# Kernel optimization log

Measured on AMD Instinct MI355X. Metric: run time of the kernel, lower is better.

Reference implementation:

```python
import jax, jax.numpy as jnp
import numpy as np
import math

NAT = 192
RCUT = 6.0
RC_ANG = 4.0
RSN_RAD = 32
RSN_ANG = 8
THETAN = 8
WIDTH = 0.5
WIDTH_ANG = 0.5
ZETA = 8.0
R0 = 0.25
BOX = 12.0


def fcut(r, rc):
    # 0.5*(1+cos(pi*r/rc)) inside cutoff, 0 outside
    return jnp.where(r <= rc, 0.5 * (1.0 + jnp.cos(jnp.pi * r / rc)), 0.0)


def app_gaussian(x):
    # power-series approximation of exp(-x): (1/(1+x/64))^64
    a = 1.0 / (1.0 + x / 64.0 + 1e-8)
    a2 = a * a; a4 = a2 * a2; a8 = a4 * a4; a16 = a8 * a8; a32 = a16 * a16
    return a32 * a32


def setup_inputs() -> dict:
    key = jax.random.key(0)
    ks = jax.random.split(key, 8)
    positions = jax.random.uniform(ks[0], (NAT, 3), dtype=jnp.float32) * BOX
    species_enc = jax.random.uniform(ks[1], (NAT,), dtype=jnp.float32)
    feat = RSN_RAD + RSN_ANG * THETAN  # 96
    W1 = jax.random.normal(ks[2], (feat, 128), dtype=jnp.float32) * (1.0 / math.sqrt(feat))
    b1 = jnp.zeros((128,), jnp.float32)
    W2 = jax.random.normal(ks[3], (128, 128), dtype=jnp.float32) * (1.0 / math.sqrt(128))
    b2 = jnp.zeros((128,), jnp.float32)
    W3 = jax.random.normal(ks[4], (128, 1), dtype=jnp.float32) * (1.0 / math.sqrt(128))
    b3 = jnp.zeros((1,), jnp.float32)
    return {"positions": positions, "species_enc": species_enc,
            "W1": W1, "b1": b1, "W2": W2, "b2": b2, "W3": W3, "b3": b3}


def reference(positions, species_enc, W1, b1, W2, b2, W3, b3):
    nat = positions.shape[0]
    # pairwise displacements r_ij = pos_i - pos_j  (matches transposed tf code)
    rij = positions[:, None, :] - positions[None, :, :]            # [i,j,3]
    rnorm = jnp.sqrt(jnp.sum(rij * rij, axis=-1) + 1e-12)           # [i,j]

    # ---- radial descriptors ----
    Rs = R0 + jnp.arange(RSN_RAD, dtype=jnp.float32) * (RCUT - R0) / RSN_RAD
    gauss = app_gaussian(WIDTH * (rnorm[:, None, :] - Rs[None, :, None]) ** 2)  # [i,s,j]
    rad = jnp.sum(species_enc[None, None, :] * gauss * fcut(rnorm, RCUT)[:, None, :], axis=-1)  # [nat, RsN_rad]

    # ---- angular (triplet) descriptors ----
    inv = 1.0 / (rnorm + 1e-20)
    u = rij * inv[:, :, None]                                       # unit vectors [i,j,3]
    cosT = jnp.einsum('ijd,ikd->ijk', u, u)                         # [i,j,k]
    sinT = jnp.sqrt(jnp.clip(1.0 - cosT * cosT, 0.0) + 1e-6)

    theta_s = jnp.arange(THETAN, dtype=jnp.float32) * jnp.pi / THETAN
    ct, st = jnp.cos(theta_s), jnp.sin(theta_s)
    norm_ang = 2.0
    # ((1 + cos(theta - theta_s)) / 2)^zeta, expanded via cos/sin of theta_s
    ang = ((1.0 + cosT[..., None] * ct + sinT[..., None] * st) / norm_ang) ** ZETA  # [i,j,k,t]

    pairw = species_enc[None, :] * fcut(rnorm, RC_ANG)              # [i,j], zero beyond rc_ang
    P = pairw[:, :, None] * pairw[:, None, :]                       # [i,j,k]

    Rs_ang = R0 + jnp.arange(RSN_ANG, dtype=jnp.float32) * (RC_ANG - R0) / RSN_ANG
    rr = 0.5 * (rnorm[:, :, None] + rnorm[:, None, :])              # [i,j,k]
    radg = app_gaussian(WIDTH_ANG * (rr[..., None] - Rs_ang) ** 2)  # [i,j,k,s]

    G_ang = jnp.einsum('ijk,ijkt,ijks->ist', P, ang, radg)          # [nat, s, t]

    desc = jnp.concatenate([rad, G_ang.reshape(nat, -1)], axis=1)   # [nat, 96]

    # per-atom MLP -> atomic energies -> total energy
    h = jnp.tanh(desc @ W1 + b1)
    h = jnp.tanh(h @ W2 + b2)
    e_at = h @ W3 + b3                                              # [nat, 1]
    return jnp.sum(e_at)
```

## Files before the change

### kernel.cpp

```cpp
#include <hip/hip_runtime.h>
#include <hip/hip_bf16.h>
#include <math.h>

#define NAT 192

__device__ __forceinline__ float app_gauss(float x) {
    float a = __builtin_amdgcn_rcpf(1.0f + x * (1.0f / 64.0f) + 1e-8f);
    a = a * a; a = a * a; a = a * a; a = a * a; a = a * a;
    return a * a;
}

__device__ __forceinline__ float fast_tanh(float x) {
    float ax = fabsf(x);
    float e = __builtin_amdgcn_exp2f(ax * 2.88539008177793f);
    float t = 1.0f - 2.0f * __builtin_amdgcn_rcpf(e + 1.0f);
    return copysignf(t, x);
}

__global__ __launch_bounds__(256) void fused_kernel(
    const float* __restrict__ pos, const float* __restrict__ spec,
    const float* __restrict__ W1, const float* __restrict__ b1,
    const float* __restrict__ W2, const float* __restrict__ b2,
    const float* __restrict__ W3, const float* __restrict__ b3,
    float* __restrict__ e_at, unsigned int* __restrict__ flags,
    float* __restrict__ out)
{
    const int i = blockIdx.x;
    const int t = threadIdx.x;
    const int lane = t & 63, wv = t >> 6;

    __shared__ float px[NAT], py[NAT], pz[NAT], sp[NAT];
    __shared__ float rn_s[NAT], w6[NAT];
    __shared__ float cux[NAT], cuy[NAT], cuz[NAT], crr[NAT], cpw[NAT];
    __shared__ int wave_cnt[4];
    __shared__ float redbuf[256];
    __shared__ float wavebuf[256];
    __shared__ float desc_s[96];
    __shared__ float part[2][128];
    __shared__ float hbuf[128];
    __shared__ float h2buf[128];
    __shared__ float final4[4];

    for (int j = t; j < NAT; j += 256) {
        px[j] = pos[3 * j + 0];
        py[j] = pos[3 * j + 1];
        pz[j] = pos[3 * j + 2];
        sp[j] = spec[j];
    }
    __syncthreads();

    const unsigned int K = __float_as_uint(px[0]);

    const float xi = px[i], yi = py[i], zi = pz[i];

    float dx = 0.f, dy = 0.f, dz = 0.f, rn = 0.f, pw = 0.f;
    bool pred = false;
    if (t < NAT) {
        dx = xi - px[t];
        dy = yi - py[t];
        dz = zi - pz[t];
        rn = sqrtf(dx * dx + dy * dy + dz * dz + 1e-12f);
        rn_s[t] = rn;
        float f6 = (rn <= 6.0f)
                       ? 0.5f * (1.0f + __builtin_amdgcn_cosf(rn * (1.0f / 12.0f)))
                       : 0.0f;
        w6[t] = sp[t] * f6;
        if (rn <= 4.0f) {
            pred = true;
            float f4 = 0.5f * (1.0f + __builtin_amdgcn_cosf(rn * 0.125f));
            pw = sp[t] * f4;
        }
    }
    unsigned long long m = __ballot(pred);
    if (lane == 0) wave_cnt[wv] = __popcll(m);
    __syncthreads();
    int base = 0;
    for (int w = 0; w < wv; ++w) base += wave_cnt[w];
    if (pred) {
        int slot = base + __popcll(m & ((1ull << lane) - 1ull));
        float inv = __builtin_amdgcn_rcpf(rn + 1e-20f);
        cux[slot] = dx * inv;
        cuy[slot] = dy * inv;
        cuz[slot] = dz * inv;
        crr[slot] = rn;
        cpw[slot] = pw;
    }
    const int nn = wave_cnt[0] + wave_cnt[1] + wave_cnt[2] + wave_cnt[3];
    __syncthreads();

    {
        const int s = t & 31, g = t >> 5;
        const float Rs = 0.25f + (float)s * 0.1796875f;
        float acc = 0.0f;
        for (int j = g; j < NAT; j += 8) {
            float d = rn_s[j] - Rs;
            acc += w6[j] * app_gauss(0.5f * d * d);
        }
        redbuf[s * 8 + g] = acc;
    }

    const float CT[8] = {1.0f, 0.92387953f, 0.70710678f, 0.38268343f,
                         -4.37113883e-08f, -0.38268343f, -0.70710678f, -0.92387953f};
    const float ST[8] = {0.0f, 0.38268343f, 0.70710678f, 0.92387953f,
                         1.0f, 0.92387953f, 0.70710678f, 0.38268343f};

    float av[64];
#pragma unroll
    for (int v = 0; v < 64; ++v) av[v] = 0.0f;

    const int T = (nn * (nn + 1)) >> 1;
    const float fn2 = 2.0f * (float)nn + 1.0f;
    for (int p = t; p < T; p += 256) {
        int a = (int)((fn2 - sqrtf(fn2 * fn2 - 8.0f * (float)p)) * 0.5f);
        if (a < 0) a = 0;
        int rs = a * nn - ((a * (a - 1)) >> 1);
        while (rs > p) { --a; rs = a * nn - ((a * (a - 1)) >> 1); }
        int rsn = (a + 1) * nn - (((a + 1) * a) >> 1);
        while (p >= rsn) { ++a; rs = rsn; rsn = (a + 1) * nn - (((a + 1) * a) >> 1); }
        int b = a + (p - rs);

        float c = cux[a] * cux[b] + cuy[a] * cuy[b] + cuz[a] * cuz[b];
        float s2 = 1.0f - c * c;
        s2 = s2 < 0.0f ? 0.0f : s2;
        float sT = sqrtf(s2 + 1e-6f);
        float P = cpw[a] * cpw[b] * ((a == b) ? 1.0f : 2.0f);
        float rr = 0.5f * (crr[a] + crr[b]);
        float angv[8];
#pragma unroll
        for (int tt = 0; tt < 8; ++tt) {
            float bse = 0.5f * (1.0f + c * CT[tt] + sT * ST[tt]);
            float b2v = bse * bse;
            float b4v = b2v * b2v;
            angv[tt] = b4v * b4v;
        }
#pragma unroll
        for (int ss = 0; ss < 8; ++ss) {
            float d = rr - (0.25f + (float)ss * 0.46875f);
            float rg = app_gauss(0.5f * d * d) * P;
#pragma unroll
            for (int tt = 0; tt < 8; ++tt)
                av[ss * 8 + tt] += rg * angv[tt];
        }
    }

#define STAGE(h)                                                         \
    {                                                                    \
        const bool up = (lane & h) != 0;                                 \
        _Pragma("unroll")                                                \
        for (int k = 0; k < h; ++k) {                                    \
            float mine   = up ? av[k + h] : av[k];                       \
            float theirs = up ? av[k] : av[k + h];                       \
            av[k] = mine + __shfl_xor(theirs, h, 64);                    \
        }                                                                \
    }
    STAGE(32) STAGE(16) STAGE(8) STAGE(4) STAGE(2) STAGE(1)
#undef STAGE
    wavebuf[wv * 64 + lane] = av[0];
    __syncthreads();

    if (t < 32) {
        float r = 0.0f;
#pragma unroll
        for (int g = 0; g < 8; ++g) r += redbuf[t * 8 + g];
        desc_s[t] = r;
    }
    if (t < 64)
        desc_s[32 + t] = wavebuf[t] + wavebuf[64 + t] + wavebuf[128 + t] + wavebuf[192 + t];
    __syncthreads();

    const int nidx = t & 127, hh = t >> 7;
    {
        float a1 = (hh == 0) ? b1[nidx] : 0.0f;
        const int f0 = hh * 48;
        for (int f = f0; f < f0 + 48; ++f) a1 += desc_s[f] * W1[f * 128 + nidx];
        part[hh][nidx] = a1;
    }
    __syncthreads();
    if (t < 128) hbuf[t] = fast_tanh(part[0][t] + part[1][t]);
    __syncthreads();
    {
        float a2 = (hh == 0) ? b2[nidx] : 0.0f;
        const int f0 = hh * 64;
        for (int f = f0; f < f0 + 64; ++f) a2 += hbuf[f] * W2[f * 128 + nidx];
        part[hh][nidx] = a2;
    }
    __syncthreads();
    if (t < 128) h2buf[t] = fast_tanh(part[0][t] + part[1][t]) * W3[t];
    __syncthreads();

    if (t < 64) {
        float v = h2buf[t] + h2buf[t + 64];
#pragma unroll
        for (int o = 32; o > 0; o >>= 1) v += __shfl_xor(v, o, 64);
        if (t == 0) {
            __hip_atomic_store(&e_at[i], v + b3[0], __ATOMIC_RELEASE,
                               __HIP_MEMORY_SCOPE_AGENT);
            __hip_atomic_store(&flags[i], K, __ATOMIC_RELEASE,
                               __HIP_MEMORY_SCOPE_AGENT);
        }
    }

    if (i == 0) {
        float v = 0.0f;
        if (t < NAT) {
            int guard = 0;
            while (__hip_atomic_load(&flags[t], __ATOMIC_ACQUIRE,
                                     __HIP_MEMORY_SCOPE_AGENT) != K) {
                __builtin_amdgcn_s_sleep(1);
                if (++guard > 10000000) break;
            }
            v = __hip_atomic_load(&e_at[t], __ATOMIC_ACQUIRE,
                                  __HIP_MEMORY_SCOPE_AGENT);
        }
#pragma unroll
        for (int o = 32; o > 0; o >>= 1) v += __shfl_xor(v, o, 64);
        if (lane == 0) final4[wv] = v;
        __syncthreads();
        if (t == 0) out[0] = final4[0] + final4[1] + final4[2] + final4[3];
        if (t < NAT)
            __hip_atomic_store(&flags[t], 0u, __ATOMIC_RELAXED,
                               __HIP_MEMORY_SCOPE_AGENT);
    }
}

extern "C" void kernel_launch(void* const* d_in, const int* in_sizes, int n_in,
                              void* d_out, int out_size, void* d_ws, size_t ws_size,
                              hipStream_t stream) {
    const float* pos  = (const float*)d_in[0];
    const float* spec = (const float*)d_in[1];
    const float* W1   = (const float*)d_in[2];
    const float* b1   = (const float*)d_in[3];
    const float* W2   = (const float*)d_in[4];
    const float* b2   = (const float*)d_in[5];
    const float* W3   = (const float*)d_in[6];
    const float* b3   = (const float*)d_in[7];

    float* e_at = (float*)d_ws;
    unsigned int* flags = (unsigned int*)((char*)d_ws + 1024);

    fused_kernel<<<NAT, 256, 0, stream>>>(pos, spec, W1, b1, W2, b2, W3, b3,
                                          e_at, flags, (float*)d_out);
}
```

Baseline: 17.20 us.

## Prefetch MLP weights into LDS asynchronously during descriptor computation

Issues async global-to-LDS loads (global_load_lds, 16 bytes per lane) for the full W1 and W2 matrices at the start of the descriptor phase, so the weight fetch overlaps the radial and angular computation. The MLP loops then read weights from LDS and are fully unrolled. This costs 112 KB of dynamic shared memory per block, which limits blocks per CU and adds LDS traffic. There is no explicit wait on the async loads before the MLP reads them, which relies on the intervening barriers and vmcnt handling.

```diff
diff --git a/kernel.cpp b/kernel.cpp
--- a/kernel.cpp
+++ b/kernel.cpp
@@ -3,6 +3,9 @@
 #include <math.h>
 
 #define NAT 192
+#define W1_FLOATS (96 * 128)
+#define W2_FLOATS (128 * 128)
+#define DYN_BYTES ((W1_FLOATS + W2_FLOATS) * 4)
 
 __device__ __forceinline__ float app_gauss(float x) {
     float a = __builtin_amdgcn_rcpf(1.0f + x * (1.0f / 64.0f) + 1e-8f);
@@ -28,6 +31,10 @@
     const int i = blockIdx.x;
     const int t = threadIdx.x;
     const int lane = t & 63, wv = t >> 6;
+
+    extern __shared__ float dynlds[];
+    float* __restrict__ W1d = dynlds;
+    float* __restrict__ W2d = dynlds + W1_FLOATS;
 
     __shared__ float px[NAT], py[NAT], pz[NAT], sp[NAT];
     __shared__ float rn_s[NAT], w6[NAT];
@@ -89,6 +96,24 @@
     __syncthreads();
 
     {
+        const int fo_lane = wv * 256 + lane * 4;
+#pragma unroll
+        for (int k = 0; k < 12; ++k) {
+            __builtin_amdgcn_global_load_lds(
+                (const __attribute__((address_space(1))) void*)(W1 + k * 1024 + fo_lane),
+                (__attribute__((address_space(3))) void*)(W1d + k * 1024 + wv * 256),
+                16, 0, 0);
+        }
+#pragma unroll
+        for (int k = 0; k < 16; ++k) {
+            __builtin_amdgcn_global_load_lds(
+                (const __attribute__((address_space(1))) void*)(W2 + k * 1024 + fo_lane),
+                (__attribute__((address_space(3))) void*)(W2d + k * 1024 + wv * 256),
+                16, 0, 0);
+        }
+    }
+
+    {
         const int s = t & 31, g = t >> 5;
         const float Rs = 0.25f + (float)s * 0.1796875f;
         float acc = 0.0f;
@@ -172,7 +197,8 @@
     {
         float a1 = (hh == 0) ? b1[nidx] : 0.0f;
         const int f0 = hh * 48;
-        for (int f = f0; f < f0 + 48; ++f) a1 += desc_s[f] * W1[f * 128 + nidx];
+#pragma unroll
+        for (int f = f0; f < f0 + 48; ++f) a1 += desc_s[f] * W1d[f * 128 + nidx];
         part[hh][nidx] = a1;
     }
     __syncthreads();
@@ -181,7 +207,8 @@
     {
         float a2 = (hh == 0) ? b2[nidx] : 0.0f;
         const int f0 = hh * 64;
-        for (int f = f0; f < f0 + 64; ++f) a2 += hbuf[f] * W2[f * 128 + nidx];
+#pragma unroll
+        for (int f = f0; f < f0 + 64; ++f) a2 += hbuf[f] * W2d[f * 128 + nidx];
         part[hh][nidx] = a2;
     }
     __syncthreads();
@@ -238,6 +265,12 @@
     float* e_at = (float*)d_ws;
     unsigned int* flags = (unsigned int*)((char*)d_ws + 1024);
 
-    fused_kernel<<<NAT, 256, 0, stream>>>(pos, spec, W1, b1, W2, b2, W3, b3,
-                                          e_at, flags, (float*)d_out);
-}
+    static_assert(DYN_BYTES == 114688, "");
+    (void)hipFuncSetAttribute((const void*)fused_kernel,
+                              hipFuncAttributeMaxDynamicSharedMemorySize,
+                              DYN_BYTES);
+
+    fused_kernel<<<NAT, 256, DYN_BYTES, stream>>>(pos, spec, W1, b1, W2, b2,
+                                                  W3, b3, e_at, flags,
+                                                  (float*)d_out);
+}
```

Measured after the change: 17.74 us. +3.1%, slower.
